# Kernel tuning notes

Measured on AMD Instinct MI355X. Metric: run time of the kernel, lower is better.

## Reference

```python
import jax, jax.numpy as jnp
import numpy as np

N_NODES = 50000
N_EDGES = 800000
D = 128          # in_feats == out_feats (residual connection)
E_DIMS = 128
NEG_SLOPE = 0.01  # F.leaky_relu default


def setup_inputs() -> dict:
    key = jax.random.key(0)
    ks = jax.random.split(key, 7)
    h = jax.random.normal(ks[0], (N_NODES, D), dtype=jnp.float32)
    edge_w = jax.random.normal(ks[1], (N_EDGES, E_DIMS), dtype=jnp.float32)
    W_self = jax.random.normal(ks[2], (D, D), dtype=jnp.float32) * (2.0 / D) ** 0.5
    W_func = jax.random.normal(ks[3], (D, D), dtype=jnp.float32) * (2.0 / D) ** 0.5
    W_att = jax.random.normal(ks[4], (1, 2 * D + E_DIMS), dtype=jnp.float32) * 0.1
    src = jax.random.randint(ks[5], (N_EDGES,), 0, N_NODES, dtype=jnp.int32)
    dst = jax.random.randint(ks[6], (N_EDGES,), 0, N_NODES, dtype=jnp.int32)
    return {"h": h, "edge_w": edge_w, "W_self": W_self, "W_func": W_func,
            "W_att": W_att, "src": src, "dst": dst}


def reference(h, edge_w, W_self, W_func, W_att, src, dst):
    N = h.shape[0]
    h_in = h
    h_s = h @ W_self.T                     # [N, D] self transform
    z = h @ W_func.T                       # [N, D] message transform

    # attention logit: leaky_relu(W_att @ [z_src, z_dst, e_w]) -- split the
    # single linear into per-node / per-edge pieces (same math, no big concat)
    wa = W_att[0]
    s_src = z @ wa[:D]                     # [N]
    s_dst = z @ wa[D:2 * D]                # [N]
    s_e = edge_w @ wa[2 * D:]              # [E]
    logits = jax.nn.leaky_relu(s_src[src] + s_dst[dst] + s_e, NEG_SLOPE)  # [E]

    # edge softmax grouped by destination node (ragged mailboxes)
    m = jax.ops.segment_max(logits, dst, num_segments=N)
    m = jnp.where(jnp.isfinite(m), m, 0.0)
    ex = jnp.exp(logits - m[dst])
    denom = jax.ops.segment_sum(ex, dst, num_segments=N)
    a = ex / jnp.maximum(denom[dst], 1e-9)                     # [E]

    # weighted scatter-sum of source messages
    agg = jax.ops.segment_sum(a[:, None] * z[src], dst, num_segments=N)  # [N, D]

    # DGL: nodes with zero in-degree keep their original ndata['h']
    deg = jax.ops.segment_sum(jnp.ones_like(logits), dst, num_segments=N)
    h_new = jnp.where(deg[:, None] > 0, h_s + agg, h_in)

    h_new = jax.nn.relu(h_new)             # relu=True
    return h_in + h_new                    # res_connection=True
```

## Files before the change

kernel.cpp:

```cpp
#include <hip/hip_runtime.h>
#include <hip/hip_bf16.h>
#include <math.h>

#define D 128
constexpr int NT = 64;

__global__ __launch_bounds__(256) void zero_int(int* __restrict__ p, int n) {
    int i = blockIdx.x * blockDim.x + threadIdx.x;
    if (i < n) p[i] = 0;
}

__global__ __launch_bounds__(256) void node_transform(
    const float* __restrict__ h, const float* __restrict__ Wf,
    const float* __restrict__ Ws, float* __restrict__ z,
    float* __restrict__ hs_out, int N)
{
    __shared__ float tile[NT * D];
    const int t = threadIdx.x;
    const int n0 = blockIdx.x * NT;
    const float* __restrict__ W = (blockIdx.y == 0) ? Wf : Ws;
    float* __restrict__ out = (blockIdx.y == 0) ? z : hs_out;
    const int nvalid = min(NT, N - n0);

    {
        const float4* __restrict__ src4 = (const float4*)(h + (size_t)n0 * D);
        float4* dst4 = (float4*)tile;
        #pragma unroll
        for (int i = 0; i < 8; ++i) {
            int idx = t + i * 256;
            float4 v = make_float4(0.f, 0.f, 0.f, 0.f);
            if ((idx >> 5) < nvalid) v = src4[idx];
            dst4[idx] = v;
        }
    }
    __syncthreads();

    const int oi = t & 63;
    const int q  = t >> 6;
    float acc0[16], acc1[16];
    #pragma unroll
    for (int n = 0; n < 16; ++n) { acc0[n] = 0.f; acc1[n] = 0.f; }

    const float* __restrict__ w0p = W + (size_t)oi * D;
    const float* __restrict__ w1p = W + (size_t)(oi + 64) * D;

    for (int kk = 0; kk < D; kk += 8) {
        float4 w00 = *(const float4*)(w0p + kk);
        float4 w01 = *(const float4*)(w0p + kk + 4);
        float4 w10 = *(const float4*)(w1p + kk);
        float4 w11 = *(const float4*)(w1p + kk + 4);
        #pragma unroll
        for (int n = 0; n < 16; ++n) {
            const float* hp = &tile[(q * 16 + n) * D + kk];
            float4 a = *(const float4*)hp;
            float4 b = *(const float4*)(hp + 4);
            acc0[n] += a.x * w00.x + a.y * w00.y + a.z * w00.z + a.w * w00.w
                     + b.x * w01.x + b.y * w01.y + b.z * w01.z + b.w * w01.w;
            acc1[n] += a.x * w10.x + a.y * w10.y + a.z * w10.z + a.w * w10.w
                     + b.x * w11.x + b.y * w11.y + b.z * w11.z + b.w * w11.w;
        }
    }

    #pragma unroll
    for (int n = 0; n < 16; ++n) {
        int node = q * 16 + n;
        if (node < nvalid) {
            size_t base = (size_t)(n0 + node) * D;
            out[base + oi]      = acc0[n];
            out[base + oi + 64] = acc1[n];
        }
    }
}

__global__ __launch_bounds__(256) void node_scores(
    const float* __restrict__ z, const float* __restrict__ wa,
    float* __restrict__ s_src, float* __restrict__ s_dst, int N)
{
    const int lane = threadIdx.x & 63;
    const int n = blockIdx.x * 4 + (threadIdx.x >> 6);
    if (n >= N) return;
    float2 zv = *(const float2*)(z + (size_t)n * D + 2 * lane);
    float a = zv.x * wa[2 * lane]     + zv.y * wa[2 * lane + 1];
    float b = zv.x * wa[D + 2 * lane] + zv.y * wa[D + 2 * lane + 1];
    #pragma unroll
    for (int off = 32; off > 0; off >>= 1) {
        a += __shfl_xor(a, off, 64);
        b += __shfl_xor(b, off, 64);
    }
    if (lane == 0) { s_src[n] = a; s_dst[n] = b; }
}

__global__ __launch_bounds__(256) void hist_kernel(
    const int* __restrict__ dst, int* __restrict__ deg, int E)
{
    int e = blockIdx.x * blockDim.x + threadIdx.x;
    if (e < E) atomicAdd(deg + dst[e], 1);
}

__global__ __launch_bounds__(256) void scan_block_sums(
    const int* __restrict__ deg, int* __restrict__ bsum, int N)
{
    __shared__ int s[256];
    int i = blockIdx.x * 256 + threadIdx.x;
    s[threadIdx.x] = (i < N) ? deg[i] : 0;
    for (int o = 128; o > 0; o >>= 1) {
        __syncthreads();
        if (threadIdx.x < o) s[threadIdx.x] += s[threadIdx.x + o];
    }
    if (threadIdx.x == 0) bsum[blockIdx.x] = s[0];
}

__global__ __launch_bounds__(256) void scan_bsum(
    const int* __restrict__ bsum, int* __restrict__ boff, int NB)
{
    __shared__ int s[256];
    int t = threadIdx.x;
    int v = (t < NB) ? bsum[t] : 0;
    s[t] = v;
    for (int o = 1; o < 256; o <<= 1) {
        __syncthreads();
        int x = (t >= o) ? s[t - o] : 0;
        __syncthreads();
        s[t] += x;
    }
    __syncthreads();
    if (t < NB) boff[t] = s[t] - v;
}

__global__ __launch_bounds__(256) void scan_final(
    const int* __restrict__ deg, const int* __restrict__ boff,
    int* __restrict__ off, int* __restrict__ cursor, int N)
{
    __shared__ int s[256];
    int t = threadIdx.x;
    int i = blockIdx.x * 256 + t;
    int v = (i < N) ? deg[i] : 0;
    s[t] = v;
    for (int o = 1; o < 256; o <<= 1) {
        __syncthreads();
        int x = (t >= o) ? s[t - o] : 0;
        __syncthreads();
        s[t] += x;
    }
    __syncthreads();
    if (i < N) {
        int ex = boff[blockIdx.x] + s[t] - v;
        off[i] = ex;
        cursor[i] = ex;
    }
}

__global__ __launch_bounds__(256) void edge_pass(
    const float* __restrict__ edge_w, const float* __restrict__ wa,
    const int* __restrict__ src, const int* __restrict__ dst,
    const float* __restrict__ s_src, const float* __restrict__ s_dst,
    int* __restrict__ cursor, int* __restrict__ src_s,
    float* __restrict__ ex_s, int E)
{
    const int lane = threadIdx.x & 63;
    const int wid = blockIdx.x * 4 + (threadIdx.x >> 6);
    const int nw  = gridDim.x * 4;
    const float we0 = wa[2 * D + 2 * lane];
    const float we1 = wa[2 * D + 2 * lane + 1];
    for (int e = wid; e < E; e += nw) {
        const int s = src[e];
        const int d = dst[e];
        float2 ew = *(const float2*)(edge_w + (size_t)e * D + 2 * lane);
        float part = ew.x * we0 + ew.y * we1;
        #pragma unroll
        for (int o = 32; o > 0; o >>= 1) part += __shfl_xor(part, o, 64);
        float logit = s_src[s] + s_dst[d] + part;
        logit = (logit > 0.f) ? logit : 0.01f * logit;
        float ex = __expf(logit);
        if (lane == 0) {
            int pos = atomicAdd(cursor + d, 1);
            src_s[pos] = s;
            ex_s[pos]  = ex;
        }
    }
}

__global__ __launch_bounds__(256) void agg_finalize(
    const int* __restrict__ off, const int* __restrict__ deg,
    const int* __restrict__ src_s, const float* __restrict__ ex_s,
    const float* __restrict__ z, const float* __restrict__ h,
    const float* __restrict__ h_s, float* __restrict__ out, int N)
{
    const int lane = threadIdx.x & 63;
    const int n = blockIdx.x * 4 + (threadIdx.x >> 6);
    if (n >= N) return;
    const int b  = off[n];
    const int dg = deg[n];
    float ax = 0.f, ay = 0.f, dsum = 0.f;
    for (int e = b; e < b + dg; ++e) {
        int s    = src_s[e];
        float ex = ex_s[e];
        dsum += ex;
        float2 zv = *(const float2*)(z + (size_t)s * D + 2 * lane);
        ax += ex * zv.x;
        ay += ex * zv.y;
    }
    float2 hv = *(const float2*)(h + (size_t)n * D + 2 * lane);
    float rx, ry;
    if (dg > 0) {
        float inv = 1.f / fmaxf(dsum, 1e-9f);
        float2 hs = *(const float2*)(h_s + (size_t)n * D + 2 * lane);
        rx = hs.x + ax * inv;
        ry = hs.y + ay * inv;
    } else {
        rx = hv.x; ry = hv.y;
    }
    rx = fmaxf(rx, 0.f); ry = fmaxf(ry, 0.f);
    float2 o = make_float2(hv.x + rx, hv.y + ry);
    *(float2*)(out + (size_t)n * D + 2 * lane) = o;
}

extern "C" void kernel_launch(void* const* d_in, const int* in_sizes, int n_in,
                              void* d_out, int out_size, void* d_ws, size_t ws_size,
                              hipStream_t stream)
{
    const float* h      = (const float*)d_in[0];
    const float* edge_w = (const float*)d_in[1];
    const float* W_self = (const float*)d_in[2];
    const float* W_func = (const float*)d_in[3];
    const float* W_att  = (const float*)d_in[4];
    const int*   src    = (const int*)d_in[5];
    const int*   dst    = (const int*)d_in[6];
    float* out = (float*)d_out;

    const int N = in_sizes[0] / D;
    const int E = in_sizes[1] / D;
    const int NB = (N + 255) / 256;

    float* z     = (float*)d_ws;
    float* ex_s  = z + (size_t)N * D;
    float* s_src = ex_s + E;
    float* s_dst = s_src + N;
    int*   src_s = (int*)(s_dst + N);
    int*   deg   = src_s + E;
    int*   off   = deg + N;
    int*   cursor= off + N;
    int*   bsum  = cursor + N;
    int*   boff  = bsum + 256;

    zero_int<<<(N + 255) / 256, 256, 0, stream>>>(deg, N);

    {
        dim3 grid((N + NT - 1) / NT, 2);
        node_transform<<<grid, 256, 0, stream>>>(h, W_func, W_self, z, out, N);
    }
    node_scores<<<(N + 3) / 4, 256, 0, stream>>>(z, W_att, s_src, s_dst, N);

    hist_kernel<<<(E + 255) / 256, 256, 0, stream>>>(dst, deg, E);
    scan_block_sums<<<NB, 256, 0, stream>>>(deg, bsum, N);
    scan_bsum<<<1, 256, 0, stream>>>(bsum, boff, NB);
    scan_final<<<NB, 256, 0, stream>>>(deg, boff, off, cursor, N);
    edge_pass<<<2048, 256, 0, stream>>>(edge_w, W_att, src, dst,
                                        s_src, s_dst, cursor, src_s, ex_s, E);

    agg_finalize<<<(N + 3) / 4, 256, 0, stream>>>(off, deg, src_s, ex_s,
                                                  z, h, out, out, N);
}
```

Before: 934.2 us.

## Split edge pass into vectorized matvec and per-thread scatter; batch agg index loads

The combined edge kernel used one 64-lane wavefront per edge, so the atomic, exp and gathers ran serialized on lane 0. The work is now split into two kernels. A 16-lane-per-edge float4 matvec computes the edge scores, and a one-thread-per-edge scatter kernel does the logits, exp and atomic bucketing. The aggregation loop now loads 64 neighbor indices and weights per wave at once and broadcasts them with shuffles instead of a dependent scalar load per edge. This adds an extra E-sized buffer round trip and one more kernel launch. The zeroing kernel is also replaced with a memset.

Measured after the change: 813.8 us. 1.15x faster.

```diff
diff --git a/kernel.cpp b/kernel.cpp
--- a/kernel.cpp
+++ b/kernel.cpp
@@ -4,11 +4,6 @@
 
 #define D 128
 constexpr int NT = 64;
-
-__global__ __launch_bounds__(256) void zero_int(int* __restrict__ p, int n) {
-    int i = blockIdx.x * blockDim.x + threadIdx.x;
-    if (i < n) p[i] = 0;
-}
 
 __global__ __launch_bounds__(256) void node_transform(
     const float* __restrict__ h, const float* __restrict__ Wf,
@@ -150,34 +145,46 @@
     }
 }
 
-__global__ __launch_bounds__(256) void edge_pass(
+__global__ __launch_bounds__(256) void edge_matvec(
     const float* __restrict__ edge_w, const float* __restrict__ wa,
+    float* __restrict__ s_e, int E)
+{
+    const int lg = threadIdx.x & 15;
+    const int g0 = (blockIdx.x * blockDim.x + threadIdx.x) >> 4;
+    const int ng = (gridDim.x * blockDim.x) >> 4;
+    const float4* wa4 = (const float4*)(wa + 2 * D);
+    const float4 w0 = wa4[2 * lg];
+    const float4 w1 = wa4[2 * lg + 1];
+    for (int e = g0; e < E; e += ng) {
+        const float4* ewp = (const float4*)(edge_w + (size_t)e * D);
+        float4 a = ewp[2 * lg];
+        float4 b = ewp[2 * lg + 1];
+        float p = a.x * w0.x + a.y * w0.y + a.z * w0.z + a.w * w0.w
+                + b.x * w1.x + b.y * w1.y + b.z * w1.z + b.w * w1.w;
+        p += __shfl_xor(p, 1, 16);
+        p += __shfl_xor(p, 2, 16);
+        p += __shfl_xor(p, 4, 16);
+        p += __shfl_xor(p, 8, 16);
+        if (lg == 0) s_e[e] = p;
+    }
+}
+
+__global__ __launch_bounds__(256) void edge_scatter(
     const int* __restrict__ src, const int* __restrict__ dst,
     const float* __restrict__ s_src, const float* __restrict__ s_dst,
-    int* __restrict__ cursor, int* __restrict__ src_s,
-    float* __restrict__ ex_s, int E)
-{
-    const int lane = threadIdx.x & 63;
-    const int wid = blockIdx.x * 4 + (threadIdx.x >> 6);
-    const int nw  = gridDim.x * 4;
-    const float we0 = wa[2 * D + 2 * lane];
-    const float we1 = wa[2 * D + 2 * lane + 1];
-    for (int e = wid; e < E; e += nw) {
-        const int s = src[e];
-        const int d = dst[e];
-        float2 ew = *(const float2*)(edge_w + (size_t)e * D + 2 * lane);
-        float part = ew.x * we0 + ew.y * we1;
-        #pragma unroll
-        for (int o = 32; o > 0; o >>= 1) part += __shfl_xor(part, o, 64);
-        float logit = s_src[s] + s_dst[d] + part;
-        logit = (logit > 0.f) ? logit : 0.01f * logit;
-        float ex = __expf(logit);
-        if (lane == 0) {
-            int pos = atomicAdd(cursor + d, 1);
-            src_s[pos] = s;
-            ex_s[pos]  = ex;
-        }
-    }
+    const float* __restrict__ s_e, int* __restrict__ cursor,
+    int* __restrict__ src_s, float* __restrict__ ex_s, int E)
+{
+    int e = blockIdx.x * blockDim.x + threadIdx.x;
+    if (e >= E) return;
+    int s = src[e];
+    int d = dst[e];
+    float logit = s_src[s] + s_dst[d] + s_e[e];
+    logit = (logit > 0.f) ? logit : 0.01f * logit;
+    float ex = __expf(logit);
+    int pos = atomicAdd(cursor + d, 1);
+    src_s[pos] = s;
+    ex_s[pos]  = ex;
 }
 
 __global__ __launch_bounds__(256) void agg_finalize(
@@ -192,13 +199,19 @@
     const int b  = off[n];
     const int dg = deg[n];
     float ax = 0.f, ay = 0.f, dsum = 0.f;
-    for (int e = b; e < b + dg; ++e) {
-        int s    = src_s[e];
-        float ex = ex_s[e];
-        dsum += ex;
-        float2 zv = *(const float2*)(z + (size_t)s * D + 2 * lane);
-        ax += ex * zv.x;
-        ay += ex * zv.y;
+    for (int base = 0; base < dg; base += 64) {
+        const int cnt = min(64, dg - base);
+        const int idx = b + base + ((lane < cnt) ? lane : 0);
+        int   sv = src_s[idx];
+        float ev = ex_s[idx];
+        for (int j = 0; j < cnt; ++j) {
+            int   s  = __shfl(sv, j, 64);
+            float ex = __shfl(ev, j, 64);
+            dsum += ex;
+            float2 zv = *(const float2*)(z + (size_t)s * D + 2 * lane);
+            ax += ex * zv.x;
+            ay += ex * zv.y;
+        }
     }
     float2 hv = *(const float2*)(h + (size_t)n * D + 2 * lane);
     float rx, ry;
@@ -234,7 +247,8 @@
 
     float* z     = (float*)d_ws;
     float* ex_s  = z + (size_t)N * D;
-    float* s_src = ex_s + E;
+    float* s_e   = ex_s + E;
+    float* s_src = s_e + E;
     float* s_dst = s_src + N;
     int*   src_s = (int*)(s_dst + N);
     int*   deg   = src_s + E;
@@ -243,20 +257,23 @@
     int*   bsum  = cursor + N;
     int*   boff  = bsum + 256;
 
-    zero_int<<<(N + 255) / 256, 256, 0, stream>>>(deg, N);
+    hipMemsetAsync(deg, 0, (size_t)N * sizeof(int), stream);
 
     {
         dim3 grid((N + NT - 1) / NT, 2);
         node_transform<<<grid, 256, 0, stream>>>(h, W_func, W_self, z, out, N);
     }
     node_scores<<<(N + 3) / 4, 256, 0, stream>>>(z, W_att, s_src, s_dst, N);
+
+    edge_matvec<<<2048, 256, 0, stream>>>(edge_w, W_att, s_e, E);
 
     hist_kernel<<<(E + 255) / 256, 256, 0, stream>>>(dst, deg, E);
     scan_block_sums<<<NB, 256, 0, stream>>>(deg, bsum, N);
     scan_bsum<<<1, 256, 0, stream>>>(bsum, boff, NB);
     scan_final<<<NB, 256, 0, stream>>>(deg, boff, off, cursor, N);
-    edge_pass<<<2048, 256, 0, stream>>>(edge_w, W_att, src, dst,
-                                        s_src, s_dst, cursor, src_s, ex_s, E);
+
+    edge_scatter<<<(E + 255) / 256, 256, 0, stream>>>(src, dst, s_src, s_dst,
+                                                      s_e, cursor, src_s, ex_s, E);
 
     agg_finalize<<<(N + 3) / 4, 256, 0, stream>>>(off, deg, src_s, ex_s,
                                                   z, h, out, out, N);
```
